# Kernel optimization log

Hardware: AMD Instinct MI355X
Metric: run time of the kernel (lower is better)

## Reference

```python
import jax, jax.numpy as jnp
import numpy as np

B, T, H = 4096, 512, 32


def setup_inputs() -> dict:
    key = jax.random.key(0)
    ks = jax.random.split(key, 7)
    s = 1.0 / np.sqrt(H)  # torch default init scale for RNN/Linear
    return {
        "x": jax.random.normal(ks[0], (B, T), dtype=jnp.float32),
        "W_ih": jax.random.uniform(ks[1], (H, 1), jnp.float32, -s, s),
        "W_hh": jax.random.uniform(ks[2], (H, H), jnp.float32, -s, s),
        "b_ih": jax.random.uniform(ks[3], (H,), jnp.float32, -s, s),
        "b_hh": jax.random.uniform(ks[4], (H,), jnp.float32, -s, s),
        "fc_w": jax.random.uniform(ks[5], (1, H), jnp.float32, -s, s),
        "fc_b": jax.random.uniform(ks[6], (1,), jnp.float32, -s, s),
    }


def reference(x, W_ih, W_hh, b_ih, b_hh, fc_w, fc_b):
    # x: [B, T] -> unsqueeze(-1) -> [B, T, 1]
    # Precompute input projections for all timesteps (vectorized):
    # xp[b, t, h] = x[b, t] * W_ih[h, 0] + b_ih[h] + b_hh[h]
    xp = x[:, :, None] * W_ih[:, 0][None, None, :] + (b_ih + b_hh)  # [B, T, H]
    h0 = jnp.zeros((x.shape[0], W_hh.shape[0]), dtype=x.dtype)

    def step(h, xp_t):
        # h_t = tanh(x_t W_ih^T + b_ih + h_{t-1} W_hh^T + b_hh)
        h_new = jnp.tanh(xp_t + h @ W_hh.T)
        return h_new, None

    h_last, _ = jax.lax.scan(step, h0, jnp.swapaxes(xp, 0, 1))  # scan over T
    out = h_last @ fc_w.T + fc_b  # [B, 1]
    return out.squeeze(-1)  # [B]
```

## Files before the change

### kernel.cpp

```cpp
#include <hip/hip_runtime.h>

#define T_LEN 512

template <int CTRL>
__device__ __forceinline__ float dppf(float v) {
    return __int_as_float(__builtin_amdgcn_update_dpp(
        0, __float_as_int(v), CTRL, 0xF, 0xF, true));
}
#define DPP_X1 0xB1
#define DPP_X2 0x4E
#define DPP_X8 0x128

template <int OFF>
__device__ __forceinline__ float swzf(float v) {
    return __int_as_float(__builtin_amdgcn_ds_swizzle(__float_as_int(v), OFF));
}

__global__ void __launch_bounds__(256) __attribute__((amdgpu_waves_per_eu(2, 2)))
rnn_fused(
    const float* __restrict__ x,
    const float* __restrict__ W_ih,
    const float* __restrict__ W_hh,
    const float* __restrict__ b_ih,
    const float* __restrict__ b_hh,
    const float* __restrict__ fc_w,
    const float* __restrict__ fc_b,
    float* __restrict__ out)
{
    __shared__ __align__(16) float xbuf[4][2][34];

    const int tid  = threadIdx.x;
    const int wv   = tid >> 6;
    const int lane = tid & 63;
    const int sub  = lane >> 5;
    const int h    = lane & 31;
    const int b    = (blockIdx.x << 3) + (wv << 1) + sub;

    float w[8][4];
#pragma unroll
    for (int ri = 0; ri < 8; ++ri) {
        const int r = (ri & 3) | ((ri & 4) << 1);
        const float* row = W_hh + (h ^ r) * 32;
#pragma unroll
        for (int mi = 0; mi < 4; ++mi) {
            const int m = ((mi & 1) << 2) | ((mi >> 1) << 4);
            w[ri][mi] = row[h ^ m];
        }
    }

    const float wih  = W_ih[h];
    const float bias = b_ih[h] + b_hh[h];
    const float* xrow = x + (size_t)b * T_LEN;

    float* xw = &xbuf[wv][sub][0];
    xw[h] = xrow[h];

    float hn = 0.0f;
#pragma unroll 1
    for (int c = 0; c < T_LEN / 32; ++c) {
        asm volatile("" : "+v"(w[0][0]), "+v"(w[0][1]), "+v"(w[0][2]), "+v"(w[0][3]),
                          "+v"(w[1][0]), "+v"(w[1][1]), "+v"(w[1][2]), "+v"(w[1][3]),
                          "+v"(w[2][0]), "+v"(w[2][1]), "+v"(w[2][2]), "+v"(w[2][3]),
                          "+v"(w[3][0]), "+v"(w[3][1]), "+v"(w[3][2]), "+v"(w[3][3]));
        asm volatile("" : "+v"(w[4][0]), "+v"(w[4][1]), "+v"(w[4][2]), "+v"(w[4][3]),
                          "+v"(w[5][0]), "+v"(w[5][1]), "+v"(w[5][2]), "+v"(w[5][3]),
                          "+v"(w[6][0]), "+v"(w[6][1]), "+v"(w[6][2]), "+v"(w[6][3]),
                          "+v"(w[7][0]), "+v"(w[7][1]), "+v"(w[7][2]), "+v"(w[7][3]));
        float xn = 0.0f;
        const bool more = (c < T_LEN / 32 - 1);
        if (more) xn = xrow[(c + 1) * 32 + h];
#pragma unroll
        for (int tc = 0; tc < 32; ++tc) {
            const float xt = xw[tc];
            const float xp = __builtin_fmaf(xt, wih, bias);

            const float b0 = hn;
            const float b1 = swzf<0x101F>(hn);
            const float b2 = swzf<0x401F>(hn);
            const float b3 = swzf<0x501F>(hn);

            float Q[8];
#pragma unroll
            for (int ri = 0; ri < 8; ++ri) {
                float q = w[ri][0] * b0;
                q = __builtin_fmaf(w[ri][1], b1, q);
                q = __builtin_fmaf(w[ri][2], b2, q);
                q = __builtin_fmaf(w[ri][3], b3, q);
                Q[ri] = q;
            }

            const float A0  = Q[0] + dppf<DPP_X1>(Q[1]);
            const float A2  = Q[2] + dppf<DPP_X1>(Q[3]);
            const float A8  = Q[4] + dppf<DPP_X1>(Q[5]);
            const float A10 = Q[6] + dppf<DPP_X1>(Q[7]);
            const float B0  = A0 + dppf<DPP_X2>(A2);
            const float B8  = A8 + dppf<DPP_X2>(A10);
            const float y   = (xp + B0) + dppf<DPP_X8>(B8);

            const float e  = __builtin_amdgcn_exp2f(y * 2.8853900817779268f);
            const float rc = __builtin_amdgcn_rcpf(e + 1.0f);
            hn = __builtin_fmaf(-2.0f, rc, 1.0f);
        }
        if (more) xw[h] = xn;
    }

    float v = hn * fc_w[h];
#pragma unroll
    for (int m = 16; m >= 1; m >>= 1) v += __shfl_xor(v, m, 64);
    if (h == 0) out[b] = v + fc_b[0];
}

extern "C" void kernel_launch(void* const* d_in, const int* in_sizes, int n_in,
                              void* d_out, int out_size, void* d_ws, size_t ws_size,
                              hipStream_t stream) {
    const float* x    = (const float*)d_in[0];
    const float* W_ih = (const float*)d_in[1];
    const float* W_hh = (const float*)d_in[2];
    const float* b_ih = (const float*)d_in[3];
    const float* b_hh = (const float*)d_in[4];
    const float* fc_w = (const float*)d_in[5];
    const float* fc_b = (const float*)d_in[6];
    float* out = (float*)d_out;

    const int B = out_size;
    dim3 grid(B / 8), block(256);
    hipLaunchKernelGGL(rnn_fused, grid, block, 0, stream,
                       x, W_ih, W_hh, b_ih, b_hh, fc_w, fc_b, out);
}
```

Measured before the change: 86.47 us.

## Pack recurrent matvec into v2f FMAs and replace swizzles with DPP/permlane16 swap

Stores the W_hh weights as packed float2 pairs so the per-step matvec can use packed FMA instructions, halving the FMA instruction count. The three ds_swizzle broadcasts of h are replaced by DPP row moves plus a permlane16 swap sum, with the weights algebraically rewritten (w0-w2, w1-w3) to consume the summed swap value. The aim is to cut the latency on the serial recurrence chain. In exchange it adds more DPP ops, and the reassociated arithmetic slightly changes rounding.

```diff
diff --git a/kernel.cpp b/kernel.cpp
--- a/kernel.cpp
+++ b/kernel.cpp
@@ -1,20 +1,33 @@
 #include <hip/hip_runtime.h>
 
 #define T_LEN 512
+
+typedef float v2f __attribute__((ext_vector_type(2)));
 
 template <int CTRL>
 __device__ __forceinline__ float dppf(float v) {
     return __int_as_float(__builtin_amdgcn_update_dpp(
         0, __float_as_int(v), CTRL, 0xF, 0xF, true));
 }
-#define DPP_X1 0xB1
-#define DPP_X2 0x4E
-#define DPP_X8 0x128
+#define DPP_X1   0xB1
+#define DPP_X2   0x4E
+#define DPP_X8   0x128
+#define DPP_X3   0x1B
+#define DPP_HM   0x141
 
-template <int OFF>
-__device__ __forceinline__ float swzf(float v) {
-    return __int_as_float(__builtin_amdgcn_ds_swizzle(__float_as_int(v), OFF));
+__device__ __forceinline__ float dpp_x4(float v) { return dppf<DPP_X3>(dppf<DPP_HM>(v)); }
+
+#if __has_builtin(__builtin_amdgcn_permlane16_swap)
+__device__ __forceinline__ float swap16_sum(float v) {
+    const unsigned i = __float_as_uint(v);
+    const auto r = __builtin_amdgcn_permlane16_swap(i, i, false, false);
+    return __uint_as_float(r[0]) + __uint_as_float(r[1]);
 }
+#else
+__device__ __forceinline__ float swap16_sum(float v) {
+    return v + __uint_as_float(__builtin_amdgcn_ds_swizzle(__float_as_uint(v), 0x401F));
+}
+#endif
 
 __global__ void __launch_bounds__(256) __attribute__((amdgpu_waves_per_eu(2, 2)))
 rnn_fused(
@@ -36,15 +49,22 @@
     const int h    = lane & 31;
     const int b    = (blockIdx.x << 3) + (wv << 1) + sub;
 
-    float w[8][4];
+    v2f wpk[4][4];
 #pragma unroll
-    for (int ri = 0; ri < 8; ++ri) {
-        const int r = (ri & 3) | ((ri & 4) << 1);
-        const float* row = W_hh + (h ^ r) * 32;
+    for (int k = 0; k < 4; ++k) {
 #pragma unroll
-        for (int mi = 0; mi < 4; ++mi) {
-            const int m = ((mi & 1) << 2) | ((mi >> 1) << 4);
-            w[ri][mi] = row[h ^ m];
+        for (int e = 0; e < 2; ++e) {
+            const int ri = 2 * k + e;
+            const int r  = (ri & 3) | ((ri & 4) << 1);
+            const float* row = W_hh + (h ^ r) * 32;
+            const float w0 = row[h];
+            const float w1 = row[h ^ 4];
+            const float w2 = row[h ^ 16];
+            const float w3 = row[h ^ 20];
+            wpk[k][0][e] = w0 - w2;
+            wpk[k][1][e] = w1 - w3;
+            wpk[k][2][e] = w2;
+            wpk[k][3][e] = w3;
         }
     }
 
@@ -58,14 +78,10 @@
     float hn = 0.0f;
 #pragma unroll 1
     for (int c = 0; c < T_LEN / 32; ++c) {
-        asm volatile("" : "+v"(w[0][0]), "+v"(w[0][1]), "+v"(w[0][2]), "+v"(w[0][3]),
-                          "+v"(w[1][0]), "+v"(w[1][1]), "+v"(w[1][2]), "+v"(w[1][3]),
-                          "+v"(w[2][0]), "+v"(w[2][1]), "+v"(w[2][2]), "+v"(w[2][3]),
-                          "+v"(w[3][0]), "+v"(w[3][1]), "+v"(w[3][2]), "+v"(w[3][3]));
-        asm volatile("" : "+v"(w[4][0]), "+v"(w[4][1]), "+v"(w[4][2]), "+v"(w[4][3]),
-                          "+v"(w[5][0]), "+v"(w[5][1]), "+v"(w[5][2]), "+v"(w[5][3]),
-                          "+v"(w[6][0]), "+v"(w[6][1]), "+v"(w[6][2]), "+v"(w[6][3]),
-                          "+v"(w[7][0]), "+v"(w[7][1]), "+v"(w[7][2]), "+v"(w[7][3]));
+        asm volatile("" : "+v"(wpk[0][0]), "+v"(wpk[0][1]), "+v"(wpk[0][2]), "+v"(wpk[0][3]),
+                          "+v"(wpk[1][0]), "+v"(wpk[1][1]), "+v"(wpk[1][2]), "+v"(wpk[1][3]));
+        asm volatile("" : "+v"(wpk[2][0]), "+v"(wpk[2][1]), "+v"(wpk[2][2]), "+v"(wpk[2][3]),
+                          "+v"(wpk[3][0]), "+v"(wpk[3][1]), "+v"(wpk[3][2]), "+v"(wpk[3][3]));
         float xn = 0.0f;
         const bool more = (c < T_LEN / 32 - 1);
         if (more) xn = xrow[(c + 1) * 32 + h];
@@ -74,28 +90,32 @@
             const float xt = xw[tc];
             const float xp = __builtin_fmaf(xt, wih, bias);
 
-            const float b0 = hn;
-            const float b1 = swzf<0x101F>(hn);
-            const float b2 = swzf<0x401F>(hn);
-            const float b3 = swzf<0x501F>(hn);
+            const float b1 = dpp_x4(hn);
+            const float s  = swap16_sum(hn);
+            const float s4 = dpp_x4(s);
 
-            float Q[8];
+            const v2f B0 = {hn, hn};
+            const v2f B1 = {b1, b1};
+            const v2f B2 = {s,  s };
+            const v2f B3 = {s4, s4};
+
+            v2f Qp[4];
 #pragma unroll
-            for (int ri = 0; ri < 8; ++ri) {
-                float q = w[ri][0] * b0;
-                q = __builtin_fmaf(w[ri][1], b1, q);
-                q = __builtin_fmaf(w[ri][2], b2, q);
-                q = __builtin_fmaf(w[ri][3], b3, q);
-                Q[ri] = q;
+            for (int k = 0; k < 4; ++k) {
+                v2f q = wpk[k][0] * B0;
+                q = __builtin_elementwise_fma(wpk[k][1], B1, q);
+                q = __builtin_elementwise_fma(wpk[k][2], B2, q);
+                q = __builtin_elementwise_fma(wpk[k][3], B3, q);
+                Qp[k] = q;
             }
 
-            const float A0  = Q[0] + dppf<DPP_X1>(Q[1]);
-            const float A2  = Q[2] + dppf<DPP_X1>(Q[3]);
-            const float A8  = Q[4] + dppf<DPP_X1>(Q[5]);
-            const float A10 = Q[6] + dppf<DPP_X1>(Q[7]);
-            const float B0  = A0 + dppf<DPP_X2>(A2);
-            const float B8  = A8 + dppf<DPP_X2>(A10);
-            const float y   = (xp + B0) + dppf<DPP_X8>(B8);
+            const float A0  = Qp[0].x + dppf<DPP_X1>(Qp[0].y);
+            const float A2  = Qp[1].x + dppf<DPP_X1>(Qp[1].y);
+            const float A8  = Qp[2].x + dppf<DPP_X1>(Qp[2].y);
+            const float A10 = Qp[3].x + dppf<DPP_X1>(Qp[3].y);
+            const float B_0 = A0 + dppf<DPP_X2>(A2);
+            const float B_8 = A8 + dppf<DPP_X2>(A10);
+            const float y   = (xp + B_0) + dppf<DPP_X8>(B_8);
 
             const float e  = __builtin_amdgcn_exp2f(y * 2.8853900817779268f);
             const float rc = __builtin_amdgcn_rcpf(e + 1.0f);
```

Result: no change. 87.99 us (+1.8%).
